# Kernel tuning notes

Measured on AMD Instinct MI355X. Metric: run time of the kernel, lower is better.

## Reference

```python
import jax, jax.numpy as jnp
import numpy as np

N_QUBITS = 8
N_LAYERS = 2
DIM = 2 ** N_QUBITS  # 256

# ---- 2x2 gate matrices (PennyLane conventions) ----

def _rx(t):
    # RX(t) = [[cos(t/2), -i sin(t/2)], [-i sin(t/2), cos(t/2)]]
    c = jnp.cos(t / 2).astype(jnp.complex64)
    s = (-1j * jnp.sin(t / 2)).astype(jnp.complex64)
    return jnp.stack([jnp.stack([c, s], -1), jnp.stack([s, c], -1)], -2)

def _ry(t):
    c = jnp.cos(t / 2).astype(jnp.complex64)
    s = jnp.sin(t / 2).astype(jnp.complex64)
    return jnp.stack([jnp.stack([c, -s], -1), jnp.stack([s, c], -1)], -2)

def _rz(t):
    e = jnp.exp(-1j * (t / 2).astype(jnp.complex64))
    z = jnp.zeros_like(e)
    return jnp.stack([jnp.stack([e, z], -1), jnp.stack([z, jnp.conj(e)], -1)], -2)

# ---- batched state-vector gate application ----
# state layout: (B, 2, 2, ..., 2); wire 0 is the most-significant axis (PennyLane default.qubit)

def _apply_1q(state, gate, wire):
    ax = 1 + wire
    state = jnp.moveaxis(state, ax, -1)
    if gate.ndim == 2:  # shared gate (trainable weights)
        state = jnp.einsum('...i,ji->...j', state, gate)
    else:               # per-sample gate (angle embedding), gate: (B,2,2)
        state = jnp.einsum('b...i,bji->b...j', state, gate)
    return jnp.moveaxis(state, -1, ax)

def _apply_cnot(state, ctrl, tgt):
    a, b = 1 + ctrl, 1 + tgt
    state = jnp.moveaxis(state, (a, b), (-2, -1))
    # flip target amplitudes where control bit = 1
    state = jnp.concatenate([state[..., 0:1, :], state[..., 1:2, ::-1]], axis=-2)
    return jnp.moveaxis(state, (-2, -1), (a, b))


def _signs():
    idx = np.arange(DIM)
    # bit of wire i in basis index (wire 0 = MSB)
    s = np.stack([1.0 - 2.0 * ((idx >> (N_QUBITS - 1 - i)) & 1)
                  for i in range(N_QUBITS)], axis=1)
    return jnp.asarray(s.astype(np.float32))  # (DIM, N_QUBITS)


def setup_inputs() -> dict:
    key = jax.random.key(0)
    k1, k2 = jax.random.split(key)
    B = 131072
    x = jax.random.normal(k1, (B, N_QUBITS), dtype=jnp.float32)
    weights = jax.random.uniform(k2, (N_LAYERS, N_QUBITS, 3), dtype=jnp.float32,
                                 minval=0.0, maxval=2.0 * np.pi)
    return {"x": x, "weights": weights}


def reference(x, weights):
    B = x.shape[0]
    state = jnp.zeros((B, DIM), jnp.complex64).at[:, 0].set(1.0)
    state = state.reshape((B,) + (2,) * N_QUBITS)
    # AngleEmbedding: RX(x[:, q]) on each wire (default rotation='X')
    for q in range(N_QUBITS):
        state = _apply_1q(state, _rx(x[:, q]), q)
    for l in range(N_LAYERS):
        for q in range(N_QUBITS):
            state = _apply_1q(state, _rx(weights[l, q, 0]), q)
            state = _apply_1q(state, _ry(weights[l, q, 1]), q)
            state = _apply_1q(state, _rz(weights[l, q, 2]), q)
        for q in range(N_QUBITS):
            state = _apply_cnot(state, q, (q + 1) % N_QUBITS)
    probs = jnp.abs(state.reshape(B, DIM)) ** 2  # (B, 256)
    return (probs @ _signs()).astype(jnp.float32)  # <Z_i> per wire, (B, 8)
```

## Files before the change

### kernel.cpp

```cpp
#include <hip/hip_runtime.h>
#include <hip/hip_bf16.h>
#include <math.h>


typedef float f2 __attribute__((ext_vector_type(2)));
typedef float f4 __attribute__((ext_vector_type(4)));
typedef short short8 __attribute__((ext_vector_type(8)));
typedef _Float16 half8 __attribute__((ext_vector_type(8)));
typedef _Float16 h2v  __attribute__((ext_vector_type(2)));

__device__ __forceinline__ f2 cmul_pk(f2 a, f2 b) {
    f2 t, d;
    asm("v_pk_mul_f32 %0, %1, %2 op_sel:[0,0] op_sel_hi:[0,1]"
        : "=v"(t) : "v"(a), "v"(b));
    asm("v_pk_fma_f32 %0, %1, %2, %3 op_sel:[1,1,0] op_sel_hi:[1,0,1] neg_lo:[1,0,0] neg_hi:[0,0,0]"
        : "=v"(d) : "v"(a), "v"(b), "v"(t));
    return d;
}

__device__ __forceinline__ f2 h2f(unsigned u) {
    h2v h; __builtin_memcpy(&h, &u, 4);
    return (f2){(float)h.x, (float)h.y};
}
__device__ __forceinline__ unsigned pkh(f2 v) {
    auto pk = __builtin_amdgcn_cvt_pkrtz(v.x, v.y);
    unsigned u; __builtin_memcpy(&u, &pk, 4);
    return u;
}

__global__ void qnn_setup(const float* __restrict__ w, float* __restrict__ p) {
    int t = threadIdx.x;
    if (t < 8) {
        int q = t;
        float cb = cosf(w[q*3+1]*0.5f), sb = sinf(w[q*3+1]*0.5f);
        float cg = cosf(w[q*3+2]*0.5f), sg = sinf(w[q*3+2]*0.5f);
        p[q] = w[q*3+0];
        float* K = p + 8 + q*8;
        K[0] = cg*cb;  K[1] = -sg*cb;
        K[2] = sg*sb;  K[3] = cg*sb;
        K[4] = cg*sb;  K[5] = sg*sb;
        K[6] = sg*cb;  K[7] = -cg*cb;
    }
    float G[8][2][2][2];
    for (int q = 0; q < 8; ++q) {
        const float* wq = w + (8+q)*3;
        float ca = cosf(wq[0]*0.5f), sa = sinf(wq[0]*0.5f);
        float cb = cosf(wq[1]*0.5f), sb = sinf(wq[1]*0.5f);
        float cg = cosf(wq[2]*0.5f), sg = sinf(wq[2]*0.5f);
        float A = cb*ca, Bv = sb*sa, C = sb*ca, D = cb*sa;
        float g00r = cg*A + sg*Bv, g00i = cg*Bv - sg*A;
        float g01r = -(cg*C + sg*D), g01i = sg*C - cg*D;
        G[q][0][0][0]=g00r;  G[q][0][0][1]=g00i;
        G[q][0][1][0]=g01r;  G[q][0][1][1]=g01i;
        G[q][1][0][0]=-g01r; G[q][1][0][1]=g01i;
        G[q][1][1][0]=g00r;  G[q][1][1][1]=-g00i;
    }
    int m = t & 15, k2 = t >> 4;
    float ar = 1.f, ai = 0.f, br = 1.f, bi = 0.f;
    for (int j = 0; j < 4; ++j) {
        int bm = (m >> (3-j)) & 1, bk = (k2 >> (3-j)) & 1;
        float gr = G[j][bm][bk][0],  gi = G[j][bm][bk][1];
        float nr = ar*gr - ai*gi, ni = ar*gi + ai*gr; ar = nr; ai = ni;
        float hr = G[4+j][bm][bk][0], hi = G[4+j][bm][bk][1];
        float mr = br*hr - bi*hi, mi = br*hi + bi*hr; br = mr; bi = mi;
    }
    __hip_bfloat16* A1 = (__hip_bfloat16*)((char*)p + 512);
    __hip_bfloat16* A2 = A1 + 512;
    __hip_bfloat16* B1 = A1 + 1024;
    __hip_bfloat16* B2 = A1 + 1536;
    int p0 = ((k2 >> 3)*16 + m)*8 + (k2 & 7);
    int k3 = k2 + 16;
    int p1 = ((k3 >> 3)*16 + m)*8 + (k3 & 7);
    A1[p0] = __float2bfloat16(ar);   A1[p1] = __float2bfloat16(-ai);
    A2[p0] = __float2bfloat16(ai);   A2[p1] = __float2bfloat16(ar);
    B1[p0] = __float2bfloat16(br);   B1[p1] = __float2bfloat16(-bi);
    B2[p0] = __float2bfloat16(bi);   B2[p1] = __float2bfloat16(br);

    const int cls[8] = {2, 0, 1, 2, 2, 2, 2, 2};
    const int msk[8] = {31, 48, 48, 48, 56, 60, 62, 63};
    _Float16* SG = (_Float16*)((char*)p + 4608);
    for (int e = t; e < 512; e += 256) {
        int tt = e >> 6, l = e & 63, n = l & 15, quad = l >> 4;
        for (int j = 0; j < 8; ++j) {
            int k  = tt*32 + quad*8 + j;
            int Lp = k >> 2, c = k & 3;
            float v = 0.f;
            if (n < 8 && c == cls[n])
                v = (__popc(msk[n] & Lp) & 1) ? -1.f : 1.f;
            SG[e*8 + j] = (_Float16)v;
        }
    }
}

#define WAVE_LDS 10240

__global__ __launch_bounds__(256, 4) void qnn_main(
        const float* __restrict__ x, const float* __restrict__ p,
        float* __restrict__ out, int B)
{
    __shared__ __align__(16) char smem[4 * WAVE_LDS];
    const int lane = threadIdx.x & 63;
    const int wid  = threadIdx.x >> 6;
    const int L = lane;
    const int b0 = (blockIdx.x * 4 + wid) * 16;
    if (b0 >= B) return;

    char* wb  = smem + wid * WAVE_LDS;
    char* Sb  = wb;
    char* Mb  = wb + 1024;
    char* THb = wb + 2304;
    char* TCb = wb + 2816;
    char* RFb = wb + 4992;
    char* Rb  = wb + 6016;
    f4*   VT  = (f4*)Rb;

    const short8* fr = (const short8*)((const char*)p + 512);
    short8 A1f = fr[L], A2f = fr[64 + L], B1f = fr[128 + L], B2f = fr[192 + L];
    const half8* sgt = (const half8*)((const char*)p + 4608);

    {
        int sI = L >> 2, qp = (L & 3) * 2;
        float2 xv  = ((const float2*)x)[(size_t)(b0 + sI)*4 + (L & 3)];
        float2 w0p = ((const float2*)p)[qp >> 1];
        const f4* Kt = (const f4*)(p + 8);
#pragma unroll
        for (int u = 0; u < 2; ++u) {
            int q = qp + u;
            float ang = (u ? xv.y : xv.x) + (u ? w0p.y : w0p.x);
            float rev = ang * 0.07957747154594767f;
            float ca = __builtin_amdgcn_cosf(rev);
            float sa = __builtin_amdgcn_sinf(rev);
            f4 Ka = Kt[q*2], Kb = Kt[q*2+1];
            f4 v;
            v.x = ca*Ka.x + sa*Ka.z;  v.y = ca*Ka.y + sa*Ka.w;
            v.z = ca*Kb.x + sa*Kb.z;  v.w = ca*Kb.y + sa*Kb.w;
            VT[sI*8 + q] = v;
        }
    }

    {
        int sI = L >> 2, j = L & 3;
        const f4* Vs = VT + sI*8;
        f4 q0v = Vs[0], q1v = Vs[1], q2v = Vs[2], q3v = Vs[3];
        f4 q4v = Vs[4], q5v = Vs[5], q6v = Vs[6], q7v = Vs[7];
        f2 V0a = {q0v.x,q0v.y}, V0b = {q0v.z,q0v.w};
        f2 V1a = {q1v.x,q1v.y}, V1b = {q1v.z,q1v.w};
        f2 V2a = {q2v.x,q2v.y}, V2b = {q2v.z,q2v.w};
        f2 V3a = {q3v.x,q3v.y}, V3b = {q3v.z,q3v.w};
        f2 V4a = {q4v.x,q4v.y}, V4b = {q4v.z,q4v.w};
        f2 V5a = {q5v.x,q5v.y}, V5b = {q5v.z,q5v.w};
        f2 V6a = {q6v.x,q6v.y}, V6b = {q6v.z,q6v.w};
        f2 V7a = {q7v.x,q7v.y}, V7b = {q7v.z,q7v.w};
        int t1 = j >> 1, t2 = j & 1;
        f2 th0 = cmul_pk(t1 ? V0b : V0a, t2 ? V1b : V1a);
        f2 th1 = cmul_pk(t1 ? V0a : V0b, t2 ? V1a : V1b);
        *(uint2*)(THb + sI*32 + j*8) = (uint2){pkh(th0), pkh(th1)};
        int col3 = j >> 1, col2 = j & 1;
        f2 v5s  = (col3 ^ col2) ? V5b : V5a;
        f2 p6_0 = cmul_pk(v5s, col2 ? V6b : V6a);
        f2 p6_1 = cmul_pk(v5s, col2 ? V6a : V6b);
        f2 V4lo = col3 ? V4b : V4a;
        f2 V4hi = col3 ? V4a : V4b;
#pragma unroll
        for (int c = 0; c < 4; ++c) {
            int c1 = c >> 1, c0 = c & 1;
            f2 cf = cmul_pk(c1 ? p6_1 : p6_0, (c1 ^ c0) ? V7b : V7a);
            f2 e0 = cmul_pk(cf, V4lo);
            f2 e1 = cmul_pk(cf, V4hi);
            *(uint2*)(TCb + sI*136 + (4*j + c)*8) = (uint2){pkh(e0), pkh(e1)};
        }
        unsigned rr[4];
#pragma unroll
        for (int r = 0; r < 4; ++r) {
            int r1 = r >> 1, r0 = r & 1;
            f2 rf = cmul_pk(((j & 1) ^ r1) ? V2b : V2a, (r1 ^ r0) ? V3b : V3a);
            rr[r] = pkh(rf);
        }
        *(uint4*)(RFb + sI*64 + j*16) = (uint4){rr[0], rr[1], rr[2], rr[3]};
    }

    const int hq  = L >> 4;
    const int col = L & 15;
    const int th_t1 = hq >> 1, th_t2 = (hq >> 1) ^ (hq & 1);
    char* THl = THb + ((th_t1*2 + th_t2)*2 + (col & 1))*4;
    char* TCl = TCb + col*8;
    char* RFl = RFb + hq*16;

    char* wSr = Sb + col*32 + hq*8;     char* wSi = wSr + 512;
    char* rS  = Sb + col*32 + (hq & 1)*16 + (hq >> 1)*512;
    char* wM  = Mb + hq*320 + col*4;
    char* rM  = Mb + col*80 + (hq & 1)*32;
    char* Rw  = Rb + L*8;
    char* Rr  = Rb + (col & 7)*528 + hq*16;
    const unsigned selM = (hq >> 1) ? 0x07060302u : 0x05040100u;
    const f4 zz = {0.f, 0.f, 0.f, 0.f};

    for (int h = 0; h < 2; ++h) {
        for (int s8 = 0; s8 < 8; ++s8) {
            const int s = h*8 + s8;
            f2 u = h2f(*(const unsigned*)(THl + s*32));
            uint2 tc = *(const uint2*)(TCl + s*136);
            uint4 rf = *(const uint4*)(RFl + s*64);
            f2 g0 = cmul_pk(u, h2f(tc.x));
            f2 g1 = cmul_pk(u, h2f(tc.y));
            f2 a0 = cmul_pk(h2f(rf.x), g0);
            f2 a1 = cmul_pk(h2f(rf.y), g1);
            f2 a2 = cmul_pk(h2f(rf.z), g0);
            f2 a3 = cmul_pk(h2f(rf.w), g1);
            unsigned r0 = __float_as_uint(a0.x)+0x8000u, r1 = __float_as_uint(a1.x)+0x8000u;
            unsigned r2 = __float_as_uint(a2.x)+0x8000u, r3 = __float_as_uint(a3.x)+0x8000u;
            unsigned i0 = __float_as_uint(a0.y)+0x8000u, i1 = __float_as_uint(a1.y)+0x8000u;
            unsigned i2 = __float_as_uint(a2.y)+0x8000u, i3 = __float_as_uint(a3.y)+0x8000u;
            uint2 pr = { __builtin_amdgcn_perm(r1, r0, 0x07060302u),
                         __builtin_amdgcn_perm(r3, r2, 0x07060302u) };
            uint2 pi = { __builtin_amdgcn_perm(i1, i0, 0x07060302u),
                         __builtin_amdgcn_perm(i3, i2, 0x07060302u) };
            *(uint2*)wSr = pr;
            *(uint2*)wSi = pi;
            short8 sfrag = *(short8*)rS;
            f4 mr = __builtin_amdgcn_mfma_f32_16x16x32_bf16(A1f, sfrag, zz, 0, 0, 0);
            f4 mi = __builtin_amdgcn_mfma_f32_16x16x32_bf16(A2f, sfrag, zz, 0, 0, 0);
            unsigned m0 = __builtin_amdgcn_perm(__float_as_uint(mi[0])+0x8000u,
                                                __float_as_uint(mr[0])+0x8000u, 0x07060302u);
            unsigned m1 = __builtin_amdgcn_perm(__float_as_uint(mi[1])+0x8000u,
                                                __float_as_uint(mr[1])+0x8000u, 0x07060302u);
            unsigned m2 = __builtin_amdgcn_perm(__float_as_uint(mi[2])+0x8000u,
                                                __float_as_uint(mr[2])+0x8000u, 0x07060302u);
            unsigned m3 = __builtin_amdgcn_perm(__float_as_uint(mi[3])+0x8000u,
                                                __float_as_uint(mr[3])+0x8000u, 0x07060302u);
            *(unsigned*)(wM +   0) = m0;  *(unsigned*)(wM +  80) = m1;
            *(unsigned*)(wM + 160) = m2;  *(unsigned*)(wM + 240) = m3;
            uint4 da = *(uint4*)rM;
            uint4 db = *(uint4*)(rM + 16);
            uint4 nf;
            nf.x = __builtin_amdgcn_perm(da.y, da.x, selM);
            nf.y = __builtin_amdgcn_perm(da.w, da.z, selM);
            nf.z = __builtin_amdgcn_perm(db.y, db.x, selM);
            nf.w = __builtin_amdgcn_perm(db.w, db.z, selM);
            short8 nfrag;
            __builtin_memcpy(&nfrag, &nf, 16);
            f4 pr4 = __builtin_amdgcn_mfma_f32_16x16x32_bf16(nfrag, B1f, zz, 0, 0, 0);
            f4 pi4 = __builtin_amdgcn_mfma_f32_16x16x32_bf16(nfrag, B2f, zz, 0, 0, 0);
            float Q0 = pr4[0]*pr4[0] + pi4[0]*pi4[0];
            float Q1 = pr4[1]*pr4[1] + pi4[1]*pi4[1];
            float Q2 = pr4[2]*pr4[2] + pi4[2]*pi4[2];
            float Q3 = pr4[3]*pr4[3] + pi4[3]*pi4[3];
            float s01 = Q0 + Q1, s23 = Q2 + Q3;
            float S00 = s01 + s23;
            float S10 = s01 - s23;
            float S11 = (Q0 - Q1) - (Q2 - Q3);
            auto h01 = __builtin_amdgcn_cvt_pkrtz(S00, S10);
            auto h23 = __builtin_amdgcn_cvt_pkrtz(S11, 0.f);
            uint2 wv;
            __builtin_memcpy(&wv.x, &h01, 4);
            __builtin_memcpy(&wv.y, &h23, 4);
            *(uint2*)(Rw + s8*528) = wv;
        }
        f4 acc = zz;
#pragma unroll
        for (int tt = 0; tt < 8; ++tt) {
            uint4 rv = *(uint4*)(Rr + tt*64);
            half8 af;
            __builtin_memcpy(&af, &rv, 16);
            acc = __builtin_amdgcn_mfma_f32_16x16x32_f16(af, sgt[tt*64 + L], acc, 0, 0, 0);
        }
        if (hq < 2 && col < 8) {
            size_t base = (size_t)(b0 + h*8 + hq*4) * 8 + col;
            out[base     ] = acc[0];
            out[base +  8] = acc[1];
            out[base + 16] = acc[2];
            out[base + 24] = acc[3];
        }
    }
}

extern "C" void kernel_launch(void* const* d_in, const int* in_sizes, int n_in,
                              void* d_out, int out_size, void* d_ws, size_t ws_size,
                              hipStream_t stream) {
    const float* x = (const float*)d_in[0];
    const float* w = (const float*)d_in[1];
    float* outp    = (float*)d_out;
    float* params  = (float*)d_ws;
    int B = in_sizes[0] / 8;

    qnn_setup<<<1, 256, 0, stream>>>(w, params);
    int blocks = (B + 63) / 64;
    qnn_main<<<blocks, 256, 0, stream>>>(x, params, outp, B);
}
```

Baseline: 92.48 us.

## Switch complex math and MFMAs to packed fp16 and shrink per-wave LDS

Complex multiplies on the state now use packed f16 instructions (v_pk_mul_f16/v_pk_fma_f16) instead of converting to f32 first. The bf16 MFMA path and its manual rounding and bit-packing are replaced by f16 MFMAs with simple pack-to-half conversions. The per-half sample loop is regrouped from 2x8 to 4x4 samples. That shrinks the result staging buffer, cutting per-wave LDS from 10240 to 8192 bytes so launch bounds can target 5 blocks per CU. The trade-off is lower arithmetic precision for the intermediate complex products and a different reduction layout.

```diff
diff --git a/kernel.cpp b/kernel.cpp
--- a/kernel.cpp
+++ b/kernel.cpp
@@ -1,13 +1,10 @@
 #include <hip/hip_runtime.h>
-#include <hip/hip_bf16.h>
 #include <math.h>
 
 
 typedef float f2 __attribute__((ext_vector_type(2)));
 typedef float f4 __attribute__((ext_vector_type(4)));
-typedef short short8 __attribute__((ext_vector_type(8)));
 typedef _Float16 half8 __attribute__((ext_vector_type(8)));
-typedef _Float16 h2v  __attribute__((ext_vector_type(2)));
 
 __device__ __forceinline__ f2 cmul_pk(f2 a, f2 b) {
     f2 t, d;
@@ -17,10 +14,13 @@
         : "=v"(d) : "v"(a), "v"(b), "v"(t));
     return d;
 }
-
-__device__ __forceinline__ f2 h2f(unsigned u) {
-    h2v h; __builtin_memcpy(&h, &u, 4);
-    return (f2){(float)h.x, (float)h.y};
+__device__ __forceinline__ unsigned cmulh(unsigned a, unsigned b) {
+    unsigned t, d;
+    asm("v_pk_mul_f16 %0, %1, %2 op_sel:[0,0] op_sel_hi:[0,1]"
+        : "=v"(t) : "v"(a), "v"(b));
+    asm("v_pk_fma_f16 %0, %1, %2, %3 op_sel:[1,1,0] op_sel_hi:[1,0,1] neg_lo:[1,0,0] neg_hi:[0,0,0]"
+        : "=v"(d) : "v"(a), "v"(b), "v"(t));
+    return d;
 }
 __device__ __forceinline__ unsigned pkh(f2 v) {
     auto pk = __builtin_amdgcn_cvt_pkrtz(v.x, v.y);
@@ -64,17 +64,17 @@
         float hr = G[4+j][bm][bk][0], hi = G[4+j][bm][bk][1];
         float mr = br*hr - bi*hi, mi = br*hi + bi*hr; br = mr; bi = mi;
     }
-    __hip_bfloat16* A1 = (__hip_bfloat16*)((char*)p + 512);
-    __hip_bfloat16* A2 = A1 + 512;
-    __hip_bfloat16* B1 = A1 + 1024;
-    __hip_bfloat16* B2 = A1 + 1536;
+    _Float16* A1 = (_Float16*)((char*)p + 512);
+    _Float16* A2 = A1 + 512;
+    _Float16* B1 = A1 + 1024;
+    _Float16* B2 = A1 + 1536;
     int p0 = ((k2 >> 3)*16 + m)*8 + (k2 & 7);
     int k3 = k2 + 16;
     int p1 = ((k3 >> 3)*16 + m)*8 + (k3 & 7);
-    A1[p0] = __float2bfloat16(ar);   A1[p1] = __float2bfloat16(-ai);
-    A2[p0] = __float2bfloat16(ai);   A2[p1] = __float2bfloat16(ar);
-    B1[p0] = __float2bfloat16(br);   B1[p1] = __float2bfloat16(-bi);
-    B2[p0] = __float2bfloat16(bi);   B2[p1] = __float2bfloat16(br);
+    A1[p0] = (_Float16)ar;   A1[p1] = (_Float16)(-ai);
+    A2[p0] = (_Float16)ai;   A2[p1] = (_Float16)ar;
+    B1[p0] = (_Float16)br;   B1[p1] = (_Float16)(-bi);
+    B2[p0] = (_Float16)bi;   B2[p1] = (_Float16)br;
 
     const int cls[8] = {2, 0, 1, 2, 2, 2, 2, 2};
     const int msk[8] = {31, 48, 48, 48, 56, 60, 62, 63};
@@ -92,9 +92,9 @@
     }
 }
 
-#define WAVE_LDS 10240
-
-__global__ __launch_bounds__(256, 4) void qnn_main(
+#define WAVE_LDS 8192
+
+__global__ __launch_bounds__(256, 5) void qnn_main(
         const float* __restrict__ x, const float* __restrict__ p,
         float* __restrict__ out, int B)
 {
@@ -114,8 +114,8 @@
     char* Rb  = wb + 6016;
     f4*   VT  = (f4*)Rb;
 
-    const short8* fr = (const short8*)((const char*)p + 512);
-    short8 A1f = fr[L], A2f = fr[64 + L], B1f = fr[128 + L], B2f = fr[192 + L];
+    const half8* fr = (const half8*)((const char*)p + 512);
+    half8 A1f = fr[L], A2f = fr[64 + L], B1f = fr[128 + L], B2f = fr[192 + L];
     const half8* sgt = (const half8*)((const char*)p + 4608);
 
     {
@@ -191,45 +191,35 @@
     char* wM  = Mb + hq*320 + col*4;
     char* rM  = Mb + col*80 + (hq & 1)*32;
     char* Rw  = Rb + L*8;
-    char* Rr  = Rb + (col & 7)*528 + hq*16;
+    char* Rr  = Rb + (col & 3)*544 + hq*16;
     const unsigned selM = (hq >> 1) ? 0x07060302u : 0x05040100u;
     const f4 zz = {0.f, 0.f, 0.f, 0.f};
 
-    for (int h = 0; h < 2; ++h) {
-        for (int s8 = 0; s8 < 8; ++s8) {
-            const int s = h*8 + s8;
-            f2 u = h2f(*(const unsigned*)(THl + s*32));
+    for (int h = 0; h < 4; ++h) {
+        for (int s4 = 0; s4 < 4; ++s4) {
+            const int s = h*4 + s4;
+            unsigned u = *(const unsigned*)(THl + s*32);
             uint2 tc = *(const uint2*)(TCl + s*136);
             uint4 rf = *(const uint4*)(RFl + s*64);
-            f2 g0 = cmul_pk(u, h2f(tc.x));
-            f2 g1 = cmul_pk(u, h2f(tc.y));
-            f2 a0 = cmul_pk(h2f(rf.x), g0);
-            f2 a1 = cmul_pk(h2f(rf.y), g1);
-            f2 a2 = cmul_pk(h2f(rf.z), g0);
-            f2 a3 = cmul_pk(h2f(rf.w), g1);
-            unsigned r0 = __float_as_uint(a0.x)+0x8000u, r1 = __float_as_uint(a1.x)+0x8000u;
-            unsigned r2 = __float_as_uint(a2.x)+0x8000u, r3 = __float_as_uint(a3.x)+0x8000u;
-            unsigned i0 = __float_as_uint(a0.y)+0x8000u, i1 = __float_as_uint(a1.y)+0x8000u;
-            unsigned i2 = __float_as_uint(a2.y)+0x8000u, i3 = __float_as_uint(a3.y)+0x8000u;
-            uint2 pr = { __builtin_amdgcn_perm(r1, r0, 0x07060302u),
-                         __builtin_amdgcn_perm(r3, r2, 0x07060302u) };
-            uint2 pi = { __builtin_amdgcn_perm(i1, i0, 0x07060302u),
-                         __builtin_amdgcn_perm(i3, i2, 0x07060302u) };
+            unsigned g0 = cmulh(u, tc.x);
+            unsigned g1 = cmulh(u, tc.y);
+            unsigned a0 = cmulh(rf.x, g0);
+            unsigned a1 = cmulh(rf.y, g1);
+            unsigned a2 = cmulh(rf.z, g0);
+            unsigned a3 = cmulh(rf.w, g1);
+            uint2 pr = { __builtin_amdgcn_perm(a1, a0, 0x05040100u),
+                         __builtin_amdgcn_perm(a3, a2, 0x05040100u) };
+            uint2 pi = { __builtin_amdgcn_perm(a1, a0, 0x07060302u),
+                         __builtin_amdgcn_perm(a3, a2, 0x07060302u) };
             *(uint2*)wSr = pr;
             *(uint2*)wSi = pi;
-            short8 sfrag = *(short8*)rS;
-            f4 mr = __builtin_amdgcn_mfma_f32_16x16x32_bf16(A1f, sfrag, zz, 0, 0, 0);
-            f4 mi = __builtin_amdgcn_mfma_f32_16x16x32_bf16(A2f, sfrag, zz, 0, 0, 0);
-            unsigned m0 = __builtin_amdgcn_perm(__float_as_uint(mi[0])+0x8000u,
-                                                __float_as_uint(mr[0])+0x8000u, 0x07060302u);
-            unsigned m1 = __builtin_amdgcn_perm(__float_as_uint(mi[1])+0x8000u,
-                                                __float_as_uint(mr[1])+0x8000u, 0x07060302u);
-            unsigned m2 = __builtin_amdgcn_perm(__float_as_uint(mi[2])+0x8000u,
-                                                __float_as_uint(mr[2])+0x8000u, 0x07060302u);
-            unsigned m3 = __builtin_amdgcn_perm(__float_as_uint(mi[3])+0x8000u,
-                                                __float_as_uint(mr[3])+0x8000u, 0x07060302u);
-            *(unsigned*)(wM +   0) = m0;  *(unsigned*)(wM +  80) = m1;
-            *(unsigned*)(wM + 160) = m2;  *(unsigned*)(wM + 240) = m3;
+            half8 sfrag = *(half8*)rS;
+            f4 mr = __builtin_amdgcn_mfma_f32_16x16x32_f16(A1f, sfrag, zz, 0, 0, 0);
+            f4 mi = __builtin_amdgcn_mfma_f32_16x16x32_f16(A2f, sfrag, zz, 0, 0, 0);
+            *(unsigned*)(wM +   0) = pkh((f2){mr[0], mi[0]});
+            *(unsigned*)(wM +  80) = pkh((f2){mr[1], mi[1]});
+            *(unsigned*)(wM + 160) = pkh((f2){mr[2], mi[2]});
+            *(unsigned*)(wM + 240) = pkh((f2){mr[3], mi[3]});
             uint4 da = *(uint4*)rM;
             uint4 db = *(uint4*)(rM + 16);
             uint4 nf;
@@ -237,10 +227,10 @@
             nf.y = __builtin_amdgcn_perm(da.w, da.z, selM);
             nf.z = __builtin_amdgcn_perm(db.y, db.x, selM);
             nf.w = __builtin_amdgcn_perm(db.w, db.z, selM);
-            short8 nfrag;
+            half8 nfrag;
             __builtin_memcpy(&nfrag, &nf, 16);
-            f4 pr4 = __builtin_amdgcn_mfma_f32_16x16x32_bf16(nfrag, B1f, zz, 0, 0, 0);
-            f4 pi4 = __builtin_amdgcn_mfma_f32_16x16x32_bf16(nfrag, B2f, zz, 0, 0, 0);
+            f4 pr4 = __builtin_amdgcn_mfma_f32_16x16x32_f16(nfrag, B1f, zz, 0, 0, 0);
+            f4 pi4 = __builtin_amdgcn_mfma_f32_16x16x32_f16(nfrag, B2f, zz, 0, 0, 0);
             float Q0 = pr4[0]*pr4[0] + pi4[0]*pi4[0];
             float Q1 = pr4[1]*pr4[1] + pi4[1]*pi4[1];
             float Q2 = pr4[2]*pr4[2] + pi4[2]*pi4[2];
@@ -249,12 +239,8 @@
             float S00 = s01 + s23;
             float S10 = s01 - s23;
             float S11 = (Q0 - Q1) - (Q2 - Q3);
-            auto h01 = __builtin_amdgcn_cvt_pkrtz(S00, S10);
-            auto h23 = __builtin_amdgcn_cvt_pkrtz(S11, 0.f);
-            uint2 wv;
-            __builtin_memcpy(&wv.x, &h01, 4);
-            __builtin_memcpy(&wv.y, &h23, 4);
-            *(uint2*)(Rw + s8*528) = wv;
+            uint2 wv = { pkh((f2){S00, S10}), pkh((f2){S11, 0.f}) };
+            *(uint2*)(Rw + s4*544) = wv;
         }
         f4 acc = zz;
 #pragma unroll
@@ -264,8 +250,8 @@
             __builtin_memcpy(&af, &rv, 16);
             acc = __builtin_amdgcn_mfma_f32_16x16x32_f16(af, sgt[tt*64 + L], acc, 0, 0, 0);
         }
-        if (hq < 2 && col < 8) {
-            size_t base = (size_t)(b0 + h*8 + hq*4) * 8 + col;
+        if (hq == 0 && col < 8) {
+            size_t base = (size_t)(b0 + h*4) * 8 + col;
             out[base     ] = acc[0];
             out[base +  8] = acc[1];
             out[base + 16] = acc[2];
```

Result: faster. 90.04 us (-2.6%).
